# Kernel optimization log

Measured on AMD Instinct MI355X. Metric: run time of the kernel, lower is better.

Reference implementation:

```python
import jax, jax.numpy as jnp
import numpy as np

N = 100000
E = 1600000
F_IN, F_HID, F_OUT = 128, 32, 2


def setup_inputs() -> dict:
    key = jax.random.key(0)
    k1, k2, k3, k4 = jax.random.split(key, 4)
    x = jax.random.normal(k1, (N, F_IN), dtype=jnp.float32)
    edge_index = jax.random.randint(k2, (2, E), 0, N, dtype=jnp.int64)
    # Glorot-style init like torch_geometric GCNConv
    W1 = jax.random.normal(k3, (F_IN, F_HID), dtype=jnp.float32) * (1.0 / np.sqrt(F_IN))
    b1 = jnp.zeros((F_HID,), dtype=jnp.float32)
    W2 = jax.random.normal(k4, (F_HID, F_OUT), dtype=jnp.float32) * (1.0 / np.sqrt(F_HID))
    b2 = jnp.zeros((F_OUT,), dtype=jnp.float32)
    return {"x": x, "edge_index": edge_index, "W1": W1, "b1": b1, "W2": W2, "b2": b2}


def _gcn_conv(x, row, col, norm, W, b):
    # GCNConv: transform, then normalized aggregate (source -> target), then bias
    h = x @ W                                   # [N, F_out]
    msg = norm[:, None] * h[row]                # gather + scale, [E+N, F_out]
    out = jax.ops.segment_sum(msg, col, num_segments=N)  # scatter-add to targets
    return out + b


def reference(x, edge_index, W1, b1, W2, b2):
    # add self-loops (GCNConv default)
    loops = jnp.arange(N, dtype=edge_index.dtype)
    row = jnp.concatenate([edge_index[0], loops])
    col = jnp.concatenate([edge_index[1], loops])
    # symmetric normalization: deg^{-1/2}[row] * deg^{-1/2}[col], deg = in-degree w/ self-loops
    deg = jax.ops.segment_sum(jnp.ones_like(col, dtype=x.dtype), col, num_segments=N)
    dinv = jnp.where(deg > 0, jax.lax.rsqrt(deg), 0.0)
    norm = dinv[row] * dinv[col]                # [E+N]

    h = _gcn_conv(x, row, col, norm, W1, b1)
    h = jax.nn.relu(h)
    h = _gcn_conv(h, row, col, norm, W2, b2)
    return jax.nn.log_softmax(h, axis=1)
```

## Files before the change

### kernel.cpp

```cpp
#include <hip/hip_runtime.h>
#include <hip/hip_bf16.h>
#include <math.h>
#include <stdint.h>


#define GNN_N 100000
#define GNN_E 1600000
#define NBUCK 391
#define CAP 4608
#define CHB 4096

typedef float fx2 __attribute__((ext_vector_type(2)));
typedef short short8x __attribute__((ext_vector_type(8)));
typedef float f32x4 __attribute__((ext_vector_type(4)));

__device__ inline uint16_t bf16_bits(float f) {
    uint32_t u = __float_as_uint(f);
    return (uint16_t)((u + 0x7fffu + ((u >> 16) & 1u)) >> 16);
}

__global__ __launch_bounds__(256) void k_bucket(const int* __restrict__ row,
                                                const int* __restrict__ col,
                                                int* __restrict__ bucket_fill,
                                                uint32_t* __restrict__ slab, int e) {
    __shared__ int hist[NBUCK];
    __shared__ int base[NBUCK];
    const int tid = threadIdx.x;
    const int e0 = blockIdx.x * CHB;
    const int m = min(CHB, e - e0);
    const bool full = (m == CHB);

    for (int i = tid; i < NBUCK; i += 256) hist[i] = 0;

    int cc[16], rr[16], pp[16];
    if (full) {
        const int4* c4 = (const int4*)(col + e0);
        const int4* r4 = (const int4*)(row + e0);
        #pragma unroll
        for (int t = 0; t < 4; ++t) {
            int4 c = c4[tid + t * 256];
            int4 r = r4[tid + t * 256];
            cc[t * 4 + 0] = c.x; cc[t * 4 + 1] = c.y;
            cc[t * 4 + 2] = c.z; cc[t * 4 + 3] = c.w;
            rr[t * 4 + 0] = r.x; rr[t * 4 + 1] = r.y;
            rr[t * 4 + 2] = r.z; rr[t * 4 + 3] = r.w;
        }
        __syncthreads();
        #pragma unroll
        for (int t = 0; t < 16; ++t)
            pp[t] = atomicAdd(&hist[cc[t] >> 8], 1);
    } else {
        __syncthreads();
        #pragma unroll
        for (int t = 0; t < 16; ++t) {
            int i = tid + t * 256;
            if (i < m) {
                cc[t] = col[e0 + i];
                rr[t] = row[e0 + i];
                pp[t] = atomicAdd(&hist[cc[t] >> 8], 1);
            }
        }
    }
    __syncthreads();
    for (int i = tid; i < NBUCK; i += 256) {
        int bb = (i + blockIdx.x * 131) % NBUCK;
        base[bb] = atomicAdd(&bucket_fill[bb], hist[bb]);
    }
    __syncthreads();
    if (full) {
        #pragma unroll
        for (int t = 0; t < 16; ++t) {
            int b = cc[t] >> 8;
            int p = base[b] + pp[t];
            if (p < CAP)
                slab[(size_t)b * CAP + p] = ((uint32_t)rr[t] << 8) | (uint32_t)(cc[t] & 255);
        }
    } else {
        #pragma unroll
        for (int t = 0; t < 16; ++t) {
            int i = tid + t * 256;
            if (i < m) {
                int b = cc[t] >> 8;
                int p = base[b] + pp[t];
                if (p < CAP)
                    slab[(size_t)b * CAP + p] = ((uint32_t)rr[t] << 8) | (uint32_t)(cc[t] & 255);
            }
        }
    }
}

__global__ __launch_bounds__(512) void k_fine(const uint32_t* __restrict__ slab,
                                              const int* __restrict__ bucket_fill,
                                              int* __restrict__ sorted_row,
                                              int* __restrict__ offsets,
                                              float* __restrict__ dinv, int n) {
    __shared__ int hist[256];
    __shared__ int excl[256];
    __shared__ int wsum[4];
    __shared__ int s_gbase;
    __shared__ uint32_t stage[CAP];
    const int tid = threadIdx.x;
    const int b0 = blockIdx.x * 2;
    const int lane = tid & 63, wave = tid >> 6;

    if (blockIdx.x == gridDim.x - 1 && tid == 511) offsets[n] = GNN_E;

    if (tid < 64) {
        int s = 0;
        for (int i = tid; i < b0; i += 64) s += bucket_fill[i];
        #pragma unroll
        for (int m = 32; m >= 1; m >>= 1) s += __shfl_xor(s, m);
        if (tid == 0) s_gbase = s;
    }
    __syncthreads();
    int gbase = s_gbase;

    for (int pass = 0; pass < 2; ++pass) {
        const int b = b0 + pass;
        if (b >= NBUCK) break;
        const int nb = min(bucket_fill[b], CAP);
        const uint32_t* sl = slab + (size_t)b * CAP;

        if (tid < 256) hist[tid] = 0;
        __syncthreads();
        uint32_t uu[9];
        int pp[9];
        #pragma unroll
        for (int j = 0; j < 9; ++j) {
            int i = tid + j * 512;
            if (i < nb) {
                uint32_t u = sl[i];
                uu[j] = u;
                pp[j] = atomicAdd(&hist[u & 255u], 1);
            }
        }
        __syncthreads();
        int v = 0, inc = 0;
        if (tid < 256) {
            v = hist[tid];
            inc = v;
            #pragma unroll
            for (int d = 1; d < 64; d <<= 1) {
                int t = __shfl_up(inc, d);
                if (lane >= d) inc += t;
            }
            if (lane == 63) wsum[wave] = inc;
        }
        __syncthreads();
        if (tid == 0) {
            int a = 0;
            #pragma unroll
            for (int w = 0; w < 4; ++w) { int t = wsum[w]; wsum[w] = a; a += t; }
        }
        __syncthreads();
        if (tid < 256) {
            int ex = inc - v + wsum[wave];
            excl[tid] = ex;
            int c = b * 256 + tid;
            if (c < n) {
                offsets[c] = gbase + ex;
                dinv[c] = rsqrtf((float)(v + 1));
            }
        }
        __syncthreads();
        #pragma unroll
        for (int j = 0; j < 9; ++j) {
            int i = tid + j * 512;
            if (i < nb)
                stage[excl[uu[j] & 255u] + pp[j]] = uu[j] >> 8;
        }
        __syncthreads();
        for (int i = tid; i < nb; i += 512)
            sorted_row[gbase + i] = (int)stage[i];
        gbase += nb;
        __syncthreads();
    }
}

#define XPAD 136
__global__ __launch_bounds__(256) void k_matmul1(const float* __restrict__ x,
                                                 const float* __restrict__ W1,
                                                 const float* __restrict__ dinv,
                                                 uint32_t* __restrict__ h1q, int n) {
    __shared__ uint16_t xs[64 * XPAD];
    __shared__ uint16_t w1t[32 * XPAD];
    const int tid = threadIdx.x;
    const int nodeBase = blockIdx.x * 64;

    for (int i = tid; i < 4096; i += 256) {
        int k = i >> 5, c = i & 31;
        w1t[c * XPAD + k] = bf16_bits(W1[i]);
    }
    {
        const float4* x4 = (const float4*)x;
        for (int i = tid; i < 64 * 32; i += 256) {
            int node = i >> 5;
            int k4 = i & 31;
            float4 v = make_float4(0.f, 0.f, 0.f, 0.f);
            if (nodeBase + node < n)
                v = x4[(size_t)(nodeBase + node) * 32 + k4];
            int b = node * XPAD + k4 * 4;
            xs[b + 0] = bf16_bits(v.x); xs[b + 1] = bf16_bits(v.y);
            xs[b + 2] = bf16_bits(v.z); xs[b + 3] = bf16_bits(v.w);
        }
    }
    __syncthreads();

    const int wave = tid >> 6;
    const int lane = tid & 63;
    const int nn = lane & 15;
    const int quad = lane >> 4;
    f32x4 acc0 = {0.f, 0.f, 0.f, 0.f};
    f32x4 acc1 = {0.f, 0.f, 0.f, 0.f};
    const int xrow = (wave * 16 + nn) * XPAD;
    #pragma unroll
    for (int s = 0; s < 4; ++s) {
        const int kof = s * 32 + quad * 8;
        short8x bfrag = *(const short8x*)&xs[xrow + kof];
        short8x a0 = *(const short8x*)&w1t[nn * XPAD + kof];
        short8x a1 = *(const short8x*)&w1t[(16 + nn) * XPAD + kof];
        acc0 = __builtin_amdgcn_mfma_f32_16x16x32_bf16(a0, bfrag, acc0, 0, 0, 0);
        acc1 = __builtin_amdgcn_mfma_f32_16x16x32_bf16(a1, bfrag, acc1, 0, 0, 0);
    }
    const int gn = nodeBase + wave * 16 + nn;
    if (gn < n) {
        float d = dinv[gn];
        int w0 = 0, w1 = 0;
        w0 = __builtin_amdgcn_cvt_pk_fp8_f32(acc0[0] * d, acc0[1] * d, w0, false);
        w0 = __builtin_amdgcn_cvt_pk_fp8_f32(acc0[2] * d, acc0[3] * d, w0, true);
        w1 = __builtin_amdgcn_cvt_pk_fp8_f32(acc1[0] * d, acc1[1] * d, w1, false);
        w1 = __builtin_amdgcn_cvt_pk_fp8_f32(acc1[2] * d, acc1[3] * d, w1, true);
        h1q[(size_t)gn * 8 + quad] = (uint32_t)w0;
        h1q[(size_t)gn * 8 + 4 + quad] = (uint32_t)w1;
    }
}

__device__ inline void fp8x16_acc(float* a, uint4 u) {
    fx2 p;
    p = __builtin_amdgcn_cvt_pk_f32_fp8(u.x, false); a[0] += p.x;  a[1] += p.y;
    p = __builtin_amdgcn_cvt_pk_f32_fp8(u.x, true);  a[2] += p.x;  a[3] += p.y;
    p = __builtin_amdgcn_cvt_pk_f32_fp8(u.y, false); a[4] += p.x;  a[5] += p.y;
    p = __builtin_amdgcn_cvt_pk_f32_fp8(u.y, true);  a[6] += p.x;  a[7] += p.y;
    p = __builtin_amdgcn_cvt_pk_f32_fp8(u.z, false); a[8] += p.x;  a[9] += p.y;
    p = __builtin_amdgcn_cvt_pk_f32_fp8(u.z, true);  a[10] += p.x; a[11] += p.y;
    p = __builtin_amdgcn_cvt_pk_f32_fp8(u.w, false); a[12] += p.x; a[13] += p.y;
    p = __builtin_amdgcn_cvt_pk_f32_fp8(u.w, true);  a[14] += p.x; a[15] += p.y;
}

__global__ __launch_bounds__(256) void k_gather1(const int* __restrict__ offsets,
                                                 const int* __restrict__ sorted_row,
                                                 const uint32_t* __restrict__ h1q,
                                                 const float* __restrict__ dinv,
                                                 const float* __restrict__ b1,
                                                 const float* __restrict__ W2,
                                                 float* __restrict__ h2s, int n) {
    __shared__ float sb1[32];
    __shared__ float sW2[64];
    const int tid = threadIdx.x;
    if (tid < 32) sb1[tid] = b1[tid];
    else if (tid < 96) sW2[tid - 32] = W2[tid - 32];
    __syncthreads();

    const int l = tid & 1;
    const int node = blockIdx.x * 128 + (tid >> 1);
    if (node >= n) return;
    const uint4* h4 = (const uint4*)h1q;
    float acc[16], acc2[16];
    #pragma unroll
    for (int j = 0; j < 16; ++j) { acc[j] = 0.f; acc2[j] = 0.f; }
    fp8x16_acc(acc, h4[(size_t)node * 2 + l]);
    const int start = offsets[node];
    const int deg = offsets[node + 1] - start;
    const int* sr = sorted_row + start;
    int k = 0;
    for (; k + 8 <= deg; k += 8) {
        int r[8];
        uint4 u[8];
        #pragma unroll
        for (int t = 0; t < 8; ++t) r[t] = sr[k + t];
        #pragma unroll
        for (int t = 0; t < 8; ++t) u[t] = h4[(size_t)r[t] * 2 + l];
        #pragma unroll
        for (int t = 0; t < 8; ++t) fp8x16_acc((t & 1) ? acc2 : acc, u[t]);
    }
    for (; k + 2 <= deg; k += 2) {
        int ra = sr[k], rb = sr[k + 1];
        uint4 ua = h4[(size_t)ra * 2 + l];
        uint4 ub = h4[(size_t)rb * 2 + l];
        fp8x16_acc(acc, ua);
        fp8x16_acc(acc2, ub);
    }
    if (k < deg)
        fp8x16_acc(acc, h4[(size_t)sr[k] * 2 + l]);
    #pragma unroll
    for (int j = 0; j < 16; ++j) acc[j] += acc2[j];

    const float dc = dinv[node];
    const int f0 = l * 16;
    float s0 = 0.f, s1 = 0.f;
    #pragma unroll
    for (int j = 0; j < 16; ++j) {
        float a = fmaxf(dc * acc[j] + sb1[f0 + j], 0.f);
        s0 += a * sW2[(f0 + j) * 2];
        s1 += a * sW2[(f0 + j) * 2 + 1];
    }
    s0 += __shfl_xor(s0, 1);
    s1 += __shfl_xor(s1, 1);
    if (l == 0) ((float2*)h2s)[node] = make_float2(dc * s0, dc * s1);
}

__global__ __launch_bounds__(256) void k_gather2(const int* __restrict__ offsets,
                                                 const int* __restrict__ sorted_row,
                                                 const float* __restrict__ h2s,
                                                 const float* __restrict__ dinv,
                                                 const float* __restrict__ b2,
                                                 float* __restrict__ out, int n) {
    const int tid = threadIdx.x;
    const int l = tid & 3;
    const int node = blockIdx.x * 64 + (tid >> 2);
    if (node >= n) return;
    const float2* h2 = (const float2*)h2s;
    float sx = 0.f, sy = 0.f;
    if (l == 0) { float2 s = h2[node]; sx = s.x; sy = s.y; }
    const int start = offsets[node];
    const int deg = offsets[node + 1] - start;
    for (int k = l; k < deg; k += 4) {
        float2 v = h2[sorted_row[start + k]];
        sx += v.x; sy += v.y;
    }
    sx += __shfl_xor(sx, 1); sx += __shfl_xor(sx, 2);
    sy += __shfl_xor(sy, 1); sy += __shfl_xor(sy, 2);
    if (l == 0) {
        float d = dinv[node];
        float v0 = d * sx + b2[0];
        float v1 = d * sy + b2[1];
        float m = fmaxf(v0, v1);
        float lg = m + logf(expf(v0 - m) + expf(v1 - m));
        ((float2*)out)[node] = make_float2(v0 - lg, v1 - lg);
    }
}

extern "C" void kernel_launch(void* const* d_in, const int* in_sizes, int n_in,
                              void* d_out, int out_size, void* d_ws, size_t ws_size,
                              hipStream_t stream) {
    const float* x  = (const float*)d_in[0];
    const int*   ei = (const int*)d_in[1];
    const float* W1 = (const float*)d_in[2];
    const float* b1 = (const float*)d_in[3];
    const float* W2 = (const float*)d_in[4];
    const float* b2 = (const float*)d_in[5];
    float* out = (float*)d_out;
    char* ws = (char*)d_ws;

    const int N = GNN_N, E = GNN_E;
    const int* row = ei;
    const int* col = ei + GNN_E;

    float*    dinv        = (float*)    ws;
    int*      offsets     = (int*)     (ws + 4ull *  100000);
    int*      bucket_fill = (int*)     (ws + 4ull *  200512);
    int*      sorted_row  = (int*)     (ws + 4ull *  201024);
    float*    h2s         = (float*)   (ws + 4ull * 1801024);
    uint32_t* h1q         = (uint32_t*)(ws + 4ull * 2001024);
    uint32_t* slab        = (uint32_t*)(ws + 4ull * 2801024);

    hipMemsetAsync(bucket_fill, 0, NBUCK * sizeof(int), stream);

    k_bucket <<<(E + CHB - 1) / CHB, 256, 0, stream>>>(row, col, bucket_fill, slab, E);
    k_fine   <<<(NBUCK + 1) / 2, 512, 0, stream>>>(slab, bucket_fill, sorted_row, offsets, dinv, N);
    k_matmul1<<<(N + 63) / 64, 256, 0, stream>>>(x, W1, dinv, h1q, N);
    k_gather1<<<(N + 127) / 128, 256, 0, stream>>>(offsets, sorted_row, h1q, dinv, b1, W2, h2s, N);
    k_gather2<<<(N + 63) / 64, 256, 0, stream>>>(offsets, sorted_row, h2s, dinv, b2, out, N);
}
```

Baseline: 163.5 us.

## Fuse fine sort with first-layer gather and compute degree via global atomics

Degree is now counted with global atomics in the bucket kernel, so the matmul can run before the fine sort. The fine-sort kernel is fused with the layer-1 gather: each block aggregates its 512 nodes using the sorted neighbour list still held in shared memory. This removes one launch and the global reread of sorted_row/offsets for layer 1. In exchange it adds 1.6M global atomics, and the gather runs on only about 196 blocks, which lowers parallelism for the heaviest phase.

```diff
diff --git a/kernel.cpp b/kernel.cpp
--- a/kernel.cpp
+++ b/kernel.cpp
@@ -22,6 +22,7 @@
 __global__ __launch_bounds__(256) void k_bucket(const int* __restrict__ row,
                                                 const int* __restrict__ col,
                                                 int* __restrict__ bucket_fill,
+                                                int* __restrict__ deg,
                                                 uint32_t* __restrict__ slab, int e) {
     __shared__ int hist[NBUCK];
     __shared__ int base[NBUCK];
@@ -45,6 +46,8 @@
             rr[t * 4 + 0] = r.x; rr[t * 4 + 1] = r.y;
             rr[t * 4 + 2] = r.z; rr[t * 4 + 3] = r.w;
         }
+        #pragma unroll
+        for (int t = 0; t < 16; ++t) atomicAdd(&deg[cc[t]], 1);
         __syncthreads();
         #pragma unroll
         for (int t = 0; t < 16; ++t)
@@ -57,6 +60,7 @@
             if (i < m) {
                 cc[t] = col[e0 + i];
                 rr[t] = row[e0 + i];
+                atomicAdd(&deg[cc[t]], 1);
                 pp[t] = atomicAdd(&hist[cc[t] >> 8], 1);
             }
         }
@@ -89,98 +93,10 @@
     }
 }
 
-__global__ __launch_bounds__(512) void k_fine(const uint32_t* __restrict__ slab,
-                                              const int* __restrict__ bucket_fill,
-                                              int* __restrict__ sorted_row,
-                                              int* __restrict__ offsets,
-                                              float* __restrict__ dinv, int n) {
-    __shared__ int hist[256];
-    __shared__ int excl[256];
-    __shared__ int wsum[4];
-    __shared__ int s_gbase;
-    __shared__ uint32_t stage[CAP];
-    const int tid = threadIdx.x;
-    const int b0 = blockIdx.x * 2;
-    const int lane = tid & 63, wave = tid >> 6;
-
-    if (blockIdx.x == gridDim.x - 1 && tid == 511) offsets[n] = GNN_E;
-
-    if (tid < 64) {
-        int s = 0;
-        for (int i = tid; i < b0; i += 64) s += bucket_fill[i];
-        #pragma unroll
-        for (int m = 32; m >= 1; m >>= 1) s += __shfl_xor(s, m);
-        if (tid == 0) s_gbase = s;
-    }
-    __syncthreads();
-    int gbase = s_gbase;
-
-    for (int pass = 0; pass < 2; ++pass) {
-        const int b = b0 + pass;
-        if (b >= NBUCK) break;
-        const int nb = min(bucket_fill[b], CAP);
-        const uint32_t* sl = slab + (size_t)b * CAP;
-
-        if (tid < 256) hist[tid] = 0;
-        __syncthreads();
-        uint32_t uu[9];
-        int pp[9];
-        #pragma unroll
-        for (int j = 0; j < 9; ++j) {
-            int i = tid + j * 512;
-            if (i < nb) {
-                uint32_t u = sl[i];
-                uu[j] = u;
-                pp[j] = atomicAdd(&hist[u & 255u], 1);
-            }
-        }
-        __syncthreads();
-        int v = 0, inc = 0;
-        if (tid < 256) {
-            v = hist[tid];
-            inc = v;
-            #pragma unroll
-            for (int d = 1; d < 64; d <<= 1) {
-                int t = __shfl_up(inc, d);
-                if (lane >= d) inc += t;
-            }
-            if (lane == 63) wsum[wave] = inc;
-        }
-        __syncthreads();
-        if (tid == 0) {
-            int a = 0;
-            #pragma unroll
-            for (int w = 0; w < 4; ++w) { int t = wsum[w]; wsum[w] = a; a += t; }
-        }
-        __syncthreads();
-        if (tid < 256) {
-            int ex = inc - v + wsum[wave];
-            excl[tid] = ex;
-            int c = b * 256 + tid;
-            if (c < n) {
-                offsets[c] = gbase + ex;
-                dinv[c] = rsqrtf((float)(v + 1));
-            }
-        }
-        __syncthreads();
-        #pragma unroll
-        for (int j = 0; j < 9; ++j) {
-            int i = tid + j * 512;
-            if (i < nb)
-                stage[excl[uu[j] & 255u] + pp[j]] = uu[j] >> 8;
-        }
-        __syncthreads();
-        for (int i = tid; i < nb; i += 512)
-            sorted_row[gbase + i] = (int)stage[i];
-        gbase += nb;
-        __syncthreads();
-    }
-}
-
 #define XPAD 136
 __global__ __launch_bounds__(256) void k_matmul1(const float* __restrict__ x,
                                                  const float* __restrict__ W1,
-                                                 const float* __restrict__ dinv,
+                                                 const int* __restrict__ deg,
                                                  uint32_t* __restrict__ h1q, int n) {
     __shared__ uint16_t xs[64 * XPAD];
     __shared__ uint16_t w1t[32 * XPAD];
@@ -224,7 +140,7 @@
     }
     const int gn = nodeBase + wave * 16 + nn;
     if (gn < n) {
-        float d = dinv[gn];
+        float d = rsqrtf((float)(deg[gn] + 1));
         int w0 = 0, w1 = 0;
         w0 = __builtin_amdgcn_cvt_pk_fp8_f32(acc0[0] * d, acc0[1] * d, w0, false);
         w0 = __builtin_amdgcn_cvt_pk_fp8_f32(acc0[2] * d, acc0[3] * d, w0, true);
@@ -247,72 +163,151 @@
     p = __builtin_amdgcn_cvt_pk_f32_fp8(u.w, true);  a[14] += p.x; a[15] += p.y;
 }
 
-__global__ __launch_bounds__(256) void k_gather1(const int* __restrict__ offsets,
-                                                 const int* __restrict__ sorted_row,
+__global__ __launch_bounds__(512) void k_fine_g1(const uint32_t* __restrict__ slab,
+                                                 const int* __restrict__ bucket_fill,
                                                  const uint32_t* __restrict__ h1q,
-                                                 const float* __restrict__ dinv,
                                                  const float* __restrict__ b1,
                                                  const float* __restrict__ W2,
+                                                 int* __restrict__ sorted_row,
+                                                 int* __restrict__ offsets,
                                                  float* __restrict__ h2s, int n) {
+    __shared__ int hist[256];
+    __shared__ int excl[256];
+    __shared__ int wsum[4];
+    __shared__ int s_gbase;
+    __shared__ uint32_t stage[CAP];
     __shared__ float sb1[32];
     __shared__ float sW2[64];
     const int tid = threadIdx.x;
-    if (tid < 32) sb1[tid] = b1[tid];
-    else if (tid < 96) sW2[tid - 32] = W2[tid - 32];
+    const int b0 = blockIdx.x * 2;
+    const int lane = tid & 63, wave = tid >> 6;
+
+    if (blockIdx.x == gridDim.x - 1 && tid == 511) offsets[n] = GNN_E;
+
+    if (tid < 64) {
+        int s = 0;
+        for (int i = tid; i < b0; i += 64) s += bucket_fill[i];
+        #pragma unroll
+        for (int m = 32; m >= 1; m >>= 1) s += __shfl_xor(s, m);
+        if (tid == 0) s_gbase = s;
+    }
+    if (tid >= 64 && tid < 96) sb1[tid - 64] = b1[tid - 64];
+    else if (tid >= 96 && tid < 160) sW2[tid - 96] = W2[tid - 96];
     __syncthreads();
-
-    const int l = tid & 1;
-    const int node = blockIdx.x * 128 + (tid >> 1);
-    if (node >= n) return;
+    int gbase = s_gbase;
     const uint4* h4 = (const uint4*)h1q;
-    float acc[16], acc2[16];
-    #pragma unroll
-    for (int j = 0; j < 16; ++j) { acc[j] = 0.f; acc2[j] = 0.f; }
-    fp8x16_acc(acc, h4[(size_t)node * 2 + l]);
-    const int start = offsets[node];
-    const int deg = offsets[node + 1] - start;
-    const int* sr = sorted_row + start;
-    int k = 0;
-    for (; k + 8 <= deg; k += 8) {
-        int r[8];
-        uint4 u[8];
-        #pragma unroll
-        for (int t = 0; t < 8; ++t) r[t] = sr[k + t];
-        #pragma unroll
-        for (int t = 0; t < 8; ++t) u[t] = h4[(size_t)r[t] * 2 + l];
-        #pragma unroll
-        for (int t = 0; t < 8; ++t) fp8x16_acc((t & 1) ? acc2 : acc, u[t]);
-    }
-    for (; k + 2 <= deg; k += 2) {
-        int ra = sr[k], rb = sr[k + 1];
-        uint4 ua = h4[(size_t)ra * 2 + l];
-        uint4 ub = h4[(size_t)rb * 2 + l];
-        fp8x16_acc(acc, ua);
-        fp8x16_acc(acc2, ub);
-    }
-    if (k < deg)
-        fp8x16_acc(acc, h4[(size_t)sr[k] * 2 + l]);
-    #pragma unroll
-    for (int j = 0; j < 16; ++j) acc[j] += acc2[j];
-
-    const float dc = dinv[node];
-    const int f0 = l * 16;
-    float s0 = 0.f, s1 = 0.f;
-    #pragma unroll
-    for (int j = 0; j < 16; ++j) {
-        float a = fmaxf(dc * acc[j] + sb1[f0 + j], 0.f);
-        s0 += a * sW2[(f0 + j) * 2];
-        s1 += a * sW2[(f0 + j) * 2 + 1];
-    }
-    s0 += __shfl_xor(s0, 1);
-    s1 += __shfl_xor(s1, 1);
-    if (l == 0) ((float2*)h2s)[node] = make_float2(dc * s0, dc * s1);
+
+    for (int pass = 0; pass < 2; ++pass) {
+        const int b = b0 + pass;
+        if (b >= NBUCK) break;
+        const int nb = min(bucket_fill[b], CAP);
+        const uint32_t* sl = slab + (size_t)b * CAP;
+
+        if (tid < 256) hist[tid] = 0;
+        __syncthreads();
+        uint32_t uu[9];
+        int pp[9];
+        #pragma unroll
+        for (int j = 0; j < 9; ++j) {
+            int i = tid + j * 512;
+            if (i < nb) {
+                uint32_t u = sl[i];
+                uu[j] = u;
+                pp[j] = atomicAdd(&hist[u & 255u], 1);
+            }
+        }
+        __syncthreads();
+        int v = 0, inc = 0;
+        if (tid < 256) {
+            v = hist[tid];
+            inc = v;
+            #pragma unroll
+            for (int d = 1; d < 64; d <<= 1) {
+                int t = __shfl_up(inc, d);
+                if (lane >= d) inc += t;
+            }
+            if (lane == 63) wsum[wave] = inc;
+        }
+        __syncthreads();
+        if (tid == 0) {
+            int a = 0;
+            #pragma unroll
+            for (int w = 0; w < 4; ++w) { int t = wsum[w]; wsum[w] = a; a += t; }
+        }
+        __syncthreads();
+        if (tid < 256) {
+            int ex = inc - v + wsum[wave];
+            excl[tid] = ex;
+            int c = b * 256 + tid;
+            if (c < n) offsets[c] = gbase + ex;
+        }
+        __syncthreads();
+        #pragma unroll
+        for (int j = 0; j < 9; ++j) {
+            int i = tid + j * 512;
+            if (i < nb)
+                stage[excl[uu[j] & 255u] + pp[j]] = uu[j] >> 8;
+        }
+        __syncthreads();
+        for (int i = tid; i < nb; i += 512)
+            sorted_row[gbase + i] = (int)stage[i];
+
+        {
+            const int nib = tid >> 1;
+            const int l = tid & 1;
+            const int gid = b * 256 + nib;
+            if (gid < n) {
+                float acc[16], acc2[16];
+                #pragma unroll
+                for (int j = 0; j < 16; ++j) { acc[j] = 0.f; acc2[j] = 0.f; }
+                fp8x16_acc(acc, h4[(size_t)gid * 2 + l]);
+                const int ex = excl[nib];
+                const int cnt = hist[nib];
+                int k = 0;
+                for (; k + 8 <= cnt; k += 8) {
+                    int r[8];
+                    uint4 u[8];
+                    #pragma unroll
+                    for (int t = 0; t < 8; ++t) r[t] = (int)stage[ex + k + t];
+                    #pragma unroll
+                    for (int t = 0; t < 8; ++t) u[t] = h4[(size_t)r[t] * 2 + l];
+                    #pragma unroll
+                    for (int t = 0; t < 8; ++t) fp8x16_acc((t & 1) ? acc2 : acc, u[t]);
+                }
+                for (; k + 2 <= cnt; k += 2) {
+                    uint4 ua = h4[(size_t)(int)stage[ex + k] * 2 + l];
+                    uint4 ub = h4[(size_t)(int)stage[ex + k + 1] * 2 + l];
+                    fp8x16_acc(acc, ua);
+                    fp8x16_acc(acc2, ub);
+                }
+                if (k < cnt)
+                    fp8x16_acc(acc, h4[(size_t)(int)stage[ex + k] * 2 + l]);
+                #pragma unroll
+                for (int j = 0; j < 16; ++j) acc[j] += acc2[j];
+
+                const float dc = rsqrtf((float)(cnt + 1));
+                const int f0 = l * 16;
+                float s0 = 0.f, s1 = 0.f;
+                #pragma unroll
+                for (int j = 0; j < 16; ++j) {
+                    float a = fmaxf(dc * acc[j] + sb1[f0 + j], 0.f);
+                    s0 += a * sW2[(f0 + j) * 2];
+                    s1 += a * sW2[(f0 + j) * 2 + 1];
+                }
+                s0 += __shfl_xor(s0, 1);
+                s1 += __shfl_xor(s1, 1);
+                if (l == 0) ((float2*)h2s)[gid] = make_float2(dc * s0, dc * s1);
+            }
+        }
+        gbase += nb;
+        __syncthreads();
+    }
 }
 
 __global__ __launch_bounds__(256) void k_gather2(const int* __restrict__ offsets,
                                                  const int* __restrict__ sorted_row,
                                                  const float* __restrict__ h2s,
-                                                 const float* __restrict__ dinv,
+                                                 const int* __restrict__ deg,
                                                  const float* __restrict__ b2,
                                                  float* __restrict__ out, int n) {
     const int tid = threadIdx.x;
@@ -323,15 +318,15 @@
     float sx = 0.f, sy = 0.f;
     if (l == 0) { float2 s = h2[node]; sx = s.x; sy = s.y; }
     const int start = offsets[node];
-    const int deg = offsets[node + 1] - start;
-    for (int k = l; k < deg; k += 4) {
+    const int dg = offsets[node + 1] - start;
+    for (int k = l; k < dg; k += 4) {
         float2 v = h2[sorted_row[start + k]];
         sx += v.x; sy += v.y;
     }
     sx += __shfl_xor(sx, 1); sx += __shfl_xor(sx, 2);
     sy += __shfl_xor(sy, 1); sy += __shfl_xor(sy, 2);
     if (l == 0) {
-        float d = dinv[node];
+        float d = rsqrtf((float)(deg[node] + 1));
         float v0 = d * sx + b2[0];
         float v1 = d * sy + b2[1];
         float m = fmaxf(v0, v1);
@@ -356,19 +351,19 @@
     const int* row = ei;
     const int* col = ei + GNN_E;
 
-    float*    dinv        = (float*)    ws;
-    int*      offsets     = (int*)     (ws + 4ull *  100000);
-    int*      bucket_fill = (int*)     (ws + 4ull *  200512);
-    int*      sorted_row  = (int*)     (ws + 4ull *  201024);
-    float*    h2s         = (float*)   (ws + 4ull * 1801024);
-    uint32_t* h1q         = (uint32_t*)(ws + 4ull * 2001024);
-    uint32_t* slab        = (uint32_t*)(ws + 4ull * 2801024);
-
-    hipMemsetAsync(bucket_fill, 0, NBUCK * sizeof(int), stream);
-
-    k_bucket <<<(E + CHB - 1) / CHB, 256, 0, stream>>>(row, col, bucket_fill, slab, E);
-    k_fine   <<<(NBUCK + 1) / 2, 512, 0, stream>>>(slab, bucket_fill, sorted_row, offsets, dinv, N);
-    k_matmul1<<<(N + 63) / 64, 256, 0, stream>>>(x, W1, dinv, h1q, N);
-    k_gather1<<<(N + 127) / 128, 256, 0, stream>>>(offsets, sorted_row, h1q, dinv, b1, W2, h2s, N);
-    k_gather2<<<(N + 63) / 64, 256, 0, stream>>>(offsets, sorted_row, h2s, dinv, b2, out, N);
-}
+    int*      deg         = (int*)      ws;
+    int*      bucket_fill = (int*)     (ws + 4ull *  100000);
+    int*      offsets     = (int*)     (ws + 4ull *  100512);
+    int*      sorted_row  = (int*)     (ws + 4ull *  200516);
+    float*    h2s         = (float*)   (ws + 4ull * 1800516);
+    uint32_t* h1q         = (uint32_t*)(ws + 4ull * 2000516);
+    uint32_t* slab        = (uint32_t*)(ws + 4ull * 2800516);
+
+    hipMemsetAsync(ws, 0, (100000 + 512) * sizeof(int), stream);
+
+    k_bucket <<<(E + CHB - 1) / CHB, 256, 0, stream>>>(row, col, bucket_fill, deg, slab, E);
+    k_matmul1<<<(N + 63) / 64, 256, 0, stream>>>(x, W1, deg, h1q, N);
+    k_fine_g1<<<(NBUCK + 1) / 2, 512, 0, stream>>>(slab, bucket_fill, h1q, b1, W2,
+                                                   sorted_row, offsets, h2s, N);
+    k_gather2<<<(N + 63) / 64, 256, 0, stream>>>(offsets, sorted_row, h2s, deg, b2, out, N);
+}
```

Result: slower. 219.2 us (+34.0%).

## Raise parallelism in bucket, fine-sort and gather1 kernels

Applied to the files above, without the earlier changes.

The bucket pass now uses 512-thread blocks over 2048-edge chunks, so each thread handles 4 edges instead of 16 and the grid has more blocks. The fine sort launches one block per bucket instead of two buckets per block, removing the serial two-pass loop. Gather1 splits each node's 32 fp8 features across 4 lanes with 8-byte loads instead of 2 lanes with 16-byte loads, which doubles the thread count and adds one more shuffle step in the reduction. The aim is more latency hiding and more blocks across the CUs, at the cost of more global atomics on bucket_fill and narrower gather loads.

```diff
diff --git a/kernel.cpp b/kernel.cpp
--- a/kernel.cpp
+++ b/kernel.cpp
@@ -8,7 +8,7 @@
 #define GNN_E 1600000
 #define NBUCK 391
 #define CAP 4608
-#define CHB 4096
+#define CHB 2048
 
 typedef float fx2 __attribute__((ext_vector_type(2)));
 typedef short short8x __attribute__((ext_vector_type(8)));
@@ -19,7 +19,7 @@
     return (uint16_t)((u + 0x7fffu + ((u >> 16) & 1u)) >> 16);
 }
 
-__global__ __launch_bounds__(256) void k_bucket(const int* __restrict__ row,
+__global__ __launch_bounds__(512) void k_bucket(const int* __restrict__ row,
                                                 const int* __restrict__ col,
                                                 int* __restrict__ bucket_fill,
                                                 uint32_t* __restrict__ slab, int e) {
@@ -30,30 +30,25 @@
     const int m = min(CHB, e - e0);
     const bool full = (m == CHB);
 
-    for (int i = tid; i < NBUCK; i += 256) hist[i] = 0;
-
-    int cc[16], rr[16], pp[16];
+    for (int i = tid; i < NBUCK; i += 512) hist[i] = 0;
+
+    int cc[4], rr[4], pp[4];
     if (full) {
         const int4* c4 = (const int4*)(col + e0);
         const int4* r4 = (const int4*)(row + e0);
-        #pragma unroll
-        for (int t = 0; t < 4; ++t) {
-            int4 c = c4[tid + t * 256];
-            int4 r = r4[tid + t * 256];
-            cc[t * 4 + 0] = c.x; cc[t * 4 + 1] = c.y;
-            cc[t * 4 + 2] = c.z; cc[t * 4 + 3] = c.w;
-            rr[t * 4 + 0] = r.x; rr[t * 4 + 1] = r.y;
-            rr[t * 4 + 2] = r.z; rr[t * 4 + 3] = r.w;
-        }
+        int4 c = c4[tid];
+        int4 r = r4[tid];
+        cc[0] = c.x; cc[1] = c.y; cc[2] = c.z; cc[3] = c.w;
+        rr[0] = r.x; rr[1] = r.y; rr[2] = r.z; rr[3] = r.w;
         __syncthreads();
         #pragma unroll
-        for (int t = 0; t < 16; ++t)
+        for (int t = 0; t < 4; ++t)
             pp[t] = atomicAdd(&hist[cc[t] >> 8], 1);
     } else {
         __syncthreads();
         #pragma unroll
-        for (int t = 0; t < 16; ++t) {
-            int i = tid + t * 256;
+        for (int t = 0; t < 4; ++t) {
+            int i = tid + t * 512;
             if (i < m) {
                 cc[t] = col[e0 + i];
                 rr[t] = row[e0 + i];
@@ -62,14 +57,14 @@
         }
     }
     __syncthreads();
-    for (int i = tid; i < NBUCK; i += 256) {
+    for (int i = tid; i < NBUCK; i += 512) {
         int bb = (i + blockIdx.x * 131) % NBUCK;
         base[bb] = atomicAdd(&bucket_fill[bb], hist[bb]);
     }
     __syncthreads();
     if (full) {
         #pragma unroll
-        for (int t = 0; t < 16; ++t) {
+        for (int t = 0; t < 4; ++t) {
             int b = cc[t] >> 8;
             int p = base[b] + pp[t];
             if (p < CAP)
@@ -77,8 +72,8 @@
         }
     } else {
         #pragma unroll
-        for (int t = 0; t < 16; ++t) {
-            int i = tid + t * 256;
+        for (int t = 0; t < 4; ++t) {
+            int i = tid + t * 512;
             if (i < m) {
                 int b = cc[t] >> 8;
                 int p = base[b] + pp[t];
@@ -100,81 +95,73 @@
     __shared__ int s_gbase;
     __shared__ uint32_t stage[CAP];
     const int tid = threadIdx.x;
-    const int b0 = blockIdx.x * 2;
+    const int b = blockIdx.x;
     const int lane = tid & 63, wave = tid >> 6;
 
-    if (blockIdx.x == gridDim.x - 1 && tid == 511) offsets[n] = GNN_E;
+    if (b == gridDim.x - 1 && tid == 511) offsets[n] = GNN_E;
 
     if (tid < 64) {
         int s = 0;
-        for (int i = tid; i < b0; i += 64) s += bucket_fill[i];
+        for (int i = tid; i < b; i += 64) s += bucket_fill[i];
         #pragma unroll
         for (int m = 32; m >= 1; m >>= 1) s += __shfl_xor(s, m);
         if (tid == 0) s_gbase = s;
     }
-    __syncthreads();
-    int gbase = s_gbase;
-
-    for (int pass = 0; pass < 2; ++pass) {
-        const int b = b0 + pass;
-        if (b >= NBUCK) break;
-        const int nb = min(bucket_fill[b], CAP);
-        const uint32_t* sl = slab + (size_t)b * CAP;
-
-        if (tid < 256) hist[tid] = 0;
-        __syncthreads();
-        uint32_t uu[9];
-        int pp[9];
-        #pragma unroll
-        for (int j = 0; j < 9; ++j) {
-            int i = tid + j * 512;
-            if (i < nb) {
-                uint32_t u = sl[i];
-                uu[j] = u;
-                pp[j] = atomicAdd(&hist[u & 255u], 1);
-            }
-        }
-        __syncthreads();
-        int v = 0, inc = 0;
-        if (tid < 256) {
-            v = hist[tid];
-            inc = v;
-            #pragma unroll
-            for (int d = 1; d < 64; d <<= 1) {
-                int t = __shfl_up(inc, d);
-                if (lane >= d) inc += t;
-            }
-            if (lane == 63) wsum[wave] = inc;
-        }
-        __syncthreads();
-        if (tid == 0) {
-            int a = 0;
-            #pragma unroll
-            for (int w = 0; w < 4; ++w) { int t = wsum[w]; wsum[w] = a; a += t; }
-        }
-        __syncthreads();
-        if (tid < 256) {
-            int ex = inc - v + wsum[wave];
-            excl[tid] = ex;
-            int c = b * 256 + tid;
-            if (c < n) {
-                offsets[c] = gbase + ex;
-                dinv[c] = rsqrtf((float)(v + 1));
-            }
-        }
-        __syncthreads();
-        #pragma unroll
-        for (int j = 0; j < 9; ++j) {
-            int i = tid + j * 512;
-            if (i < nb)
-                stage[excl[uu[j] & 255u] + pp[j]] = uu[j] >> 8;
-        }
-        __syncthreads();
-        for (int i = tid; i < nb; i += 512)
-            sorted_row[gbase + i] = (int)stage[i];
-        gbase += nb;
-        __syncthreads();
-    }
+    if (tid >= 64 && tid < 320) hist[tid - 64] = 0;
+    __syncthreads();
+    const int gbase = s_gbase;
+    const int nb = min(bucket_fill[b], CAP);
+    const uint32_t* sl = slab + (size_t)b * CAP;
+
+    uint32_t uu[9];
+    int pp[9];
+    #pragma unroll
+    for (int j = 0; j < 9; ++j) {
+        int i = tid + j * 512;
+        if (i < nb) {
+            uint32_t u = sl[i];
+            uu[j] = u;
+            pp[j] = atomicAdd(&hist[u & 255u], 1);
+        }
+    }
+    __syncthreads();
+    int v = 0, inc = 0;
+    if (tid < 256) {
+        v = hist[tid];
+        inc = v;
+        #pragma unroll
+        for (int d = 1; d < 64; d <<= 1) {
+            int t = __shfl_up(inc, d);
+            if (lane >= d) inc += t;
+        }
+        if (lane == 63) wsum[wave] = inc;
+    }
+    __syncthreads();
+    if (tid == 0) {
+        int a = 0;
+        #pragma unroll
+        for (int w = 0; w < 4; ++w) { int t = wsum[w]; wsum[w] = a; a += t; }
+    }
+    __syncthreads();
+    if (tid < 256) {
+        int ex = inc - v + wsum[wave];
+        excl[tid] = ex;
+        int c = b * 256 + tid;
+        if (c < n) {
+            offsets[c] = gbase + ex;
+            dinv[c] = rsqrtf((float)(v + 1));
+        }
+    }
+    __syncthreads();
+    #pragma unroll
+    for (int j = 0; j < 9; ++j) {
+        int i = tid + j * 512;
+        if (i < nb)
+            stage[excl[uu[j] & 255u] + pp[j]] = uu[j] >> 8;
+    }
+    __syncthreads();
+    for (int i = tid; i < nb; i += 512)
+        sorted_row[gbase + i] = (int)stage[i];
 }
 
 #define XPAD 136
@@ -235,16 +222,12 @@
     }
 }
 
-__device__ inline void fp8x16_acc(float* a, uint4 u) {
+__device__ inline void fp8x8_acc(float* a, uint2 u) {
     fx2 p;
     p = __builtin_amdgcn_cvt_pk_f32_fp8(u.x, false); a[0] += p.x;  a[1] += p.y;
     p = __builtin_amdgcn_cvt_pk_f32_fp8(u.x, true);  a[2] += p.x;  a[3] += p.y;
     p = __builtin_amdgcn_cvt_pk_f32_fp8(u.y, false); a[4] += p.x;  a[5] += p.y;
     p = __builtin_amdgcn_cvt_pk_f32_fp8(u.y, true);  a[6] += p.x;  a[7] += p.y;
-    p = __builtin_amdgcn_cvt_pk_f32_fp8(u.z, false); a[8] += p.x;  a[9] += p.y;
-    p = __builtin_amdgcn_cvt_pk_f32_fp8(u.z, true);  a[10] += p.x; a[11] += p.y;
-    p = __builtin_amdgcn_cvt_pk_f32_fp8(u.w, false); a[12] += p.x; a[13] += p.y;
-    p = __builtin_amdgcn_cvt_pk_f32_fp8(u.w, true);  a[14] += p.x; a[15] += p.y;
 }
 
 __global__ __launch_bounds__(256) void k_gather1(const int* __restrict__ offsets,
@@ -261,51 +244,51 @@
     else if (tid < 96) sW2[tid - 32] = W2[tid - 32];
     __syncthreads();
 
-    const int l = tid & 1;
-    const int node = blockIdx.x * 128 + (tid >> 1);
+    const int l = tid & 3;
+    const int node = blockIdx.x * 64 + (tid >> 2);
     if (node >= n) return;
-    const uint4* h4 = (const uint4*)h1q;
-    float acc[16], acc2[16];
-    #pragma unroll
-    for (int j = 0; j < 16; ++j) { acc[j] = 0.f; acc2[j] = 0.f; }
-    fp8x16_acc(acc, h4[(size_t)node * 2 + l]);
+    const uint2* h2p = (const uint2*)h1q;
+    float acc[8], acc2[8];
+    #pragma unroll
+    for (int j = 0; j < 8; ++j) { acc[j] = 0.f; acc2[j] = 0.f; }
+    fp8x8_acc(acc, h2p[(size_t)node * 4 + l]);
     const int start = offsets[node];
     const int deg = offsets[node + 1] - start;
     const int* sr = sorted_row + start;
     int k = 0;
     for (; k + 8 <= deg; k += 8) {
         int r[8];
-        uint4 u[8];
+        uint2 u[8];
         #pragma unroll
         for (int t = 0; t < 8; ++t) r[t] = sr[k + t];
         #pragma unroll
-        for (int t = 0; t < 8; ++t) u[t] = h4[(size_t)r[t] * 2 + l];
-        #pragma unroll
-        for (int t = 0; t < 8; ++t) fp8x16_acc((t & 1) ? acc2 : acc, u[t]);
+        for (int t = 0; t < 8; ++t) u[t] = h2p[(size_t)r[t] * 4 + l];
+        #pragma unroll
+        for (int t = 0; t < 8; ++t) fp8x8_acc((t & 1) ? acc2 : acc, u[t]);
     }
     for (; k + 2 <= deg; k += 2) {
         int ra = sr[k], rb = sr[k + 1];
-        uint4 ua = h4[(size_t)ra * 2 + l];
-        uint4 ub = h4[(size_t)rb * 2 + l];
-        fp8x16_acc(acc, ua);
-        fp8x16_acc(acc2, ub);
+        uint2 ua = h2p[(size_t)ra * 4 + l];
+        uint2 ub = h2p[(size_t)rb * 4 + l];
+        fp8x8_acc(acc, ua);
+        fp8x8_acc(acc2, ub);
     }
     if (k < deg)
-        fp8x16_acc(acc, h4[(size_t)sr[k] * 2 + l]);
-    #pragma unroll
-    for (int j = 0; j < 16; ++j) acc[j] += acc2[j];
+        fp8x8_acc(acc, h2p[(size_t)sr[k] * 4 + l]);
+    #pragma unroll
+    for (int j = 0; j < 8; ++j) acc[j] += acc2[j];
 
     const float dc = dinv[node];
-    const int f0 = l * 16;
+    const int f0 = l * 8;
     float s0 = 0.f, s1 = 0.f;
     #pragma unroll
-    for (int j = 0; j < 16; ++j) {
+    for (int j = 0; j < 8; ++j) {
         float a = fmaxf(dc * acc[j] + sb1[f0 + j], 0.f);
         s0 += a * sW2[(f0 + j) * 2];
         s1 += a * sW2[(f0 + j) * 2 + 1];
     }
-    s0 += __shfl_xor(s0, 1);
-    s1 += __shfl_xor(s1, 1);
+    s0 += __shfl_xor(s0, 1); s0 += __shfl_xor(s0, 2);
+    s1 += __shfl_xor(s1, 1); s1 += __shfl_xor(s1, 2);
     if (l == 0) ((float2*)h2s)[node] = make_float2(dc * s0, dc * s1);
 }
 
@@ -364,11 +347,11 @@
     uint32_t* h1q         = (uint32_t*)(ws + 4ull * 2001024);
     uint32_t* slab        = (uint32_t*)(ws + 4ull * 2801024);
 
-    hipMemsetAsync(bucket_fill, 0, NBUCK * sizeof(int), stream);
-
-    k_bucket <<<(E + CHB - 1) / CHB, 256, 0, stream>>>(row, col, bucket_fill, slab, E);
-    k_fine   <<<(NBUCK + 1) / 2, 512, 0, stream>>>(slab, bucket_fill, sorted_row, offsets, dinv, N);
+    hipMemsetAsync(bucket_fill, 0, 512 * sizeof(int), stream);
+
+    k_bucket <<<(E + CHB - 1) / CHB, 512, 0, stream>>>(row, col, bucket_fill, slab, E);
+    k_fine   <<<NBUCK, 512, 0, stream>>>(slab, bucket_fill, sorted_row, offsets, dinv, N);
     k_matmul1<<<(N + 63) / 64, 256, 0, stream>>>(x, W1, dinv, h1q, N);
-    k_gather1<<<(N + 127) / 128, 256, 0, stream>>>(offsets, sorted_row, h1q, dinv, b1, W2, h2s, N);
+    k_gather1<<<(N + 63) / 64, 256, 0, stream>>>(offsets, sorted_row, h1q, dinv, b1, W2, h2s, N);
     k_gather2<<<(N + 63) / 64, 256, 0, stream>>>(offsets, sorted_row, h2s, dinv, b2, out, N);
 }
```

Result: slower. 167.8 us (+2.6%).
